# Kernel optimization log

Measured on AMD Instinct MI355X. Metric: run time of the kernel, lower is better.

The kernel has to match this reference:

```python
import jax, jax.numpy as jnp
import numpy as np

DIM = 1024
HEAD_SIZE = 128
B, N = 4, 4096

def setup_inputs() -> dict:
    key = jax.random.key(0)
    kx, kq, kk, kv = jax.random.split(key, 4)
    s = (1.0 / DIM) ** 0.5  # ~ torch Linear init scale
    return {
        "x": jax.random.normal(kx, (B, N, DIM), dtype=jnp.float32),
        "Wq": jax.random.uniform(kq, (HEAD_SIZE, DIM), dtype=jnp.float32, minval=-s, maxval=s),
        "Wk": jax.random.uniform(kk, (HEAD_SIZE, DIM), dtype=jnp.float32, minval=-s, maxval=s),
        "Wv": jax.random.uniform(kv, (HEAD_SIZE, DIM), dtype=jnp.float32, minval=-s, maxval=s),
    }

def reference(x, Wq, Wk, Wv):
    # x: [B, N, dim]; W*: [head_size, dim] (torch Linear convention y = x @ W.T)
    q = jnp.einsum('bnd,hd->bnh', x, Wq)
    k = jnp.einsum('bnd,hd->bnh', x, Wk)
    v = jnp.einsum('bnd,hd->bnh', x, Wv)
    scale = DIM ** (-0.5)  # NOTE: original scales by dim**-0.5, not head_size
    scores = jnp.einsum('bnh,bmh->bnm', q, k) * scale  # [B, N, N]
    weights = jax.nn.softmax(scores, axis=-1)
    context = jnp.einsum('bnm,bmh->bnh', weights, v)  # [B, N, head_size]
    return context
```

## Files before the change

### kernel.cpp

```cpp
#include <hip/hip_runtime.h>

using bf16x8   = __attribute__((ext_vector_type(8))) __bf16;
using f32x4    = __attribute__((ext_vector_type(4))) float;
using floatv4  = __attribute__((ext_vector_type(4))) float;
using ushortv8 = __attribute__((ext_vector_type(8))) unsigned short;

#define N_SEQ 4096
#define N_B   4
#define DIMK  1024
#define HS    128
#define ROWS  (N_B * N_SEQ)
#define KVB   32

__device__ __forceinline__ unsigned short f2bf(float f) {
    unsigned u = __builtin_bit_cast(unsigned, f);
    u += 0x7FFFu + ((u >> 16) & 1u);
    return (unsigned short)(u >> 16);
}

__device__ __forceinline__ void gload16(const unsigned short* g, unsigned short* l) {
    __builtin_amdgcn_global_load_lds(
        (const __attribute__((address_space(1))) unsigned int*)g,
        (__attribute__((address_space(3))) unsigned int*)l, 16, 0, 0);
}

__global__ __launch_bounds__(256) void cast_kernel(
    const float* __restrict__ X,
    const float* __restrict__ Wq,
    const float* __restrict__ Wk,
    const float* __restrict__ Wv,
    unsigned short* __restrict__ Xb,
    unsigned short* __restrict__ Wb)
{
    const int blk = blockIdx.x;
    const float* src;
    unsigned short* dst;
    size_t off;
    if (blk < 8192) {
        src = X; dst = Xb; off = (size_t)blk * 2048;
    } else {
        int wblk = blk - 8192;
        int z = wblk >> 6;
        src = (z == 0) ? Wq : (z == 1) ? Wk : Wv;
        dst = Wb + (size_t)z * (HS * DIMK);
        off = (size_t)(wblk & 63) * 2048;
    }
    size_t i = off + (size_t)threadIdx.x * 8;
    floatv4 a = *reinterpret_cast<const floatv4*>(src + i);
    floatv4 b = *reinterpret_cast<const floatv4*>(src + i + 4);
    ushortv8 o = { f2bf(a.x), f2bf(a.y), f2bf(a.z), f2bf(a.w),
                   f2bf(b.x), f2bf(b.y), f2bf(b.z), f2bf(b.w) };
    *reinterpret_cast<ushortv8*>(dst + i) = o;
}

__global__ __launch_bounds__(256, 3) void proj_kernel(
    const unsigned short* __restrict__ Xb,
    const unsigned short* __restrict__ Wb,
    unsigned short* __restrict__ Qb,
    unsigned short* __restrict__ Kb,
    unsigned short* __restrict__ Vt)
{
    const int z = blockIdx.y;
    const unsigned short* __restrict__ Wz = Wb + (size_t)z * (HS * DIMK);
    const int row0 = blockIdx.x * 64;
    __shared__ unsigned short smem[2 * 64 * 64 + 2 * 128 * 64];
    unsigned short* Xs0 = smem;
    unsigned short* Ws0 = smem + 2 * 64 * 64;
    const int tid = threadIdx.x;
    const int wv = tid >> 6, lane = tid & 63;
    const int lr = lane & 15, lg = lane >> 4;

    f32x4 acc[4][2] = {};

    auto stage = [&](int buf, int k0) {
        #pragma unroll
        for (int i = 0; i < 2; ++i) {
            int g = wv * 2 + i;
            int r = g * 8 + (lane >> 3);
            int sp = (lane & 7) ^ (r & 7);
            gload16(Xb + (size_t)(row0 + r) * DIMK + k0 + sp * 8,
                    Xs0 + buf * (64 * 64) + g * 8 * 64);
        }
        #pragma unroll
        for (int i = 0; i < 4; ++i) {
            int g = wv * 4 + i;
            int r = g * 8 + (lane >> 3);
            int sp = (lane & 7) ^ (r & 7);
            gload16(Wz + (size_t)r * DIMK + k0 + sp * 8,
                    Ws0 + buf * (128 * 64) + g * 8 * 64);
        }
    };

    stage(0, 0);
    __syncthreads();
    for (int ks = 0; ks < DIMK / 64; ++ks) {
        const int cur = ks & 1;
        if (ks < DIMK / 64 - 1) stage(cur ^ 1, (ks + 1) * 64);
        const unsigned short* Xc = Xs0 + cur * (64 * 64);
        const unsigned short* Wc = Ws0 + cur * (128 * 64);
        bf16x8 af[4][2], bfr[2][2];
        #pragma unroll
        for (int mi = 0; mi < 4; ++mi)
            #pragma unroll
            for (int kk = 0; kk < 2; ++kk)
                af[mi][kk] = *reinterpret_cast<const bf16x8*>(
                    &Xc[(mi * 16 + lr) * 64 + (((kk * 4 + lg) ^ (lr & 7)) * 8)]);
        #pragma unroll
        for (int ni = 0; ni < 2; ++ni)
            #pragma unroll
            for (int kk = 0; kk < 2; ++kk)
                bfr[ni][kk] = *reinterpret_cast<const bf16x8*>(
                    &Wc[(wv * 32 + ni * 16 + lr) * 64 + (((kk * 4 + lg) ^ (lr & 7)) * 8)]);
        #pragma unroll
        for (int kk = 0; kk < 2; ++kk)
            #pragma unroll
            for (int mi = 0; mi < 4; ++mi)
                #pragma unroll
                for (int ni = 0; ni < 2; ++ni)
                    acc[mi][ni] = __builtin_amdgcn_mfma_f32_16x16x32_bf16(
                        af[mi][kk], bfr[ni][kk], acc[mi][ni], 0, 0, 0);
        __syncthreads();
    }

    if (z < 2) {
        unsigned short* O = (z == 0) ? Qb : Kb;
        #pragma unroll
        for (int mi = 0; mi < 4; ++mi) {
            int rowb = row0 + mi * 16 + lg * 4;
            #pragma unroll
            for (int ni = 0; ni < 2; ++ni) {
                int col = wv * 32 + ni * 16 + lr;
                #pragma unroll
                for (int r = 0; r < 4; ++r)
                    O[(size_t)(rowb + r) * HS + col] = f2bf(acc[mi][ni][r]);
            }
        }
    } else {
        unsigned short* Cs = smem;
        #pragma unroll
        for (int mi = 0; mi < 4; ++mi)
            #pragma unroll
            for (int ni = 0; ni < 2; ++ni)
                #pragma unroll
                for (int r = 0; r < 4; ++r)
                    Cs[(mi * 16 + lg * 4 + r) * 132 + wv * 32 + ni * 16 + lr] = f2bf(acc[mi][ni][r]);
        __syncthreads();
        const int b  = row0 >> 12;
        const int n0 = row0 & (N_SEQ - 1);
        #pragma unroll
        for (int i = 0; i < 4; ++i) {
            int idx = tid + i * 256;
            int d = idx >> 3, c8 = idx & 7;
            ushortv8 v;
            #pragma unroll
            for (int j = 0; j < 8; ++j)
                v[j] = Cs[(c8 * 8 + j) * 132 + d];
            *reinterpret_cast<ushortv8*>(Vt + (size_t)b * HS * N_SEQ + (size_t)d * N_SEQ + n0 + c8 * 8) = v;
        }
    }
}

__global__ __launch_bounds__(256, 2) void attn_kernel(
    const unsigned short* __restrict__ Qb,
    const unsigned short* __restrict__ Kb,
    const unsigned short* __restrict__ Vt,
    float* __restrict__ part,
    float* __restrict__ plsum,
    int S)
{
    const int qblk  = blockIdx.x;
    const int split = blockIdx.y;
    const int tid = threadIdx.x;
    const int wv = tid >> 6, lane = tid & 63;
    const int lr = lane & 15, lg = lane >> 4;
    const int b    = qblk >> 5;
    const int row0 = (qblk & 31) * 128 + wv * 32;

    __shared__ unsigned short Ks[2][KVB * 128];
    __shared__ unsigned short Vs[2][128 * KVB];
    __shared__ unsigned short Ps[4][32 * 40];
    unsigned short* ps = Ps[wv];

    bf16x8 qf[2][4];
    #pragma unroll
    for (int m = 0; m < 2; ++m) {
        const unsigned short* qp = Qb + ((size_t)b * N_SEQ + row0 + m * 16 + lr) * HS + lg * 8;
        #pragma unroll
        for (int kk = 0; kk < 4; ++kk)
            qf[m][kk] = *reinterpret_cast<const bf16x8*>(qp + kk * 32);
    }

    const int kvlen = N_SEQ / S;
    const int nt = kvlen / KVB;
    const int kv_begin = split * kvlen;
    const unsigned short* Kbb = Kb + (size_t)b * N_SEQ * HS;
    const unsigned short* Vbb = Vt + (size_t)b * HS * N_SEQ;

    auto stage = [&](int buf, int kv0) {
        #pragma unroll
        for (int i = 0; i < 2; ++i) {
            int g = wv * 2 + i;
            int r = g * 4 + (lane >> 4);
            int sp = (lane & 15) ^ (r & 7);
            gload16(Kbb + (size_t)(kv0 + r) * HS + sp * 8, &Ks[buf][g * 4 * 128]);
        }
        #pragma unroll
        for (int i = 0; i < 2; ++i) {
            int g = wv * 2 + i;
            int r = g * 16 + (lane >> 2);
            int sp = (lane & 3) ^ ((r >> 1) & 3);
            gload16(Vbb + (size_t)r * N_SEQ + kv0 + sp * 8, &Vs[buf][g * 16 * KVB]);
        }
    };

    f32x4 ctx[2][8] = {};
    f32x4 lacc[2] = {};
    const ushortv8 ones_u = {0x3F80,0x3F80,0x3F80,0x3F80,0x3F80,0x3F80,0x3F80,0x3F80};
    const bf16x8 onesf = __builtin_bit_cast(bf16x8, ones_u);
    const float CEXP = 0.045084220027780106f;

    stage(0, kv_begin);
    __syncthreads();
    for (int t = 0; t < nt; ++t) {
        const int cur = t & 1;
        if (t + 1 < nt) stage(cur ^ 1, kv_begin + (t + 1) * KVB);

        #pragma unroll
        for (int ni = 0; ni < 2; ++ni) {
            bf16x8 kf[4];
            #pragma unroll
            for (int kk = 0; kk < 4; ++kk)
                kf[kk] = *reinterpret_cast<const bf16x8*>(
                    &Ks[cur][(ni * 16 + lr) * 128 + (((kk * 4 + lg) ^ (lr & 7)) * 8)]);
            #pragma unroll
            for (int m = 0; m < 2; ++m) {
                f32x4 sv = {0.f, 0.f, 0.f, 0.f};
                #pragma unroll
                for (int kk = 0; kk < 4; ++kk)
                    sv = __builtin_amdgcn_mfma_f32_16x16x32_bf16(qf[m][kk], kf[kk], sv, 0, 0, 0);
                #pragma unroll
                for (int r = 0; r < 4; ++r) {
                    float pe = exp2f(sv[r] * CEXP);
                    ps[(m * 16 + lg * 4 + r) * 40 + ni * 16 + lr] = f2bf(pe);
                }
            }
        }

        bf16x8 pf0 = *reinterpret_cast<const bf16x8*>(&ps[lr * 40 + lg * 8]);
        bf16x8 pf1 = *reinterpret_cast<const bf16x8*>(&ps[(16 + lr) * 40 + lg * 8]);
        lacc[0] = __builtin_amdgcn_mfma_f32_16x16x32_bf16(pf0, onesf, lacc[0], 0, 0, 0);
        lacc[1] = __builtin_amdgcn_mfma_f32_16x16x32_bf16(pf1, onesf, lacc[1], 0, 0, 0);
        #pragma unroll
        for (int di = 0; di < 8; ++di) {
            bf16x8 vf = *reinterpret_cast<const bf16x8*>(
                &Vs[cur][(di * 16 + lr) * KVB + ((lg ^ ((lr >> 1) & 3)) * 8)]);
            ctx[0][di] = __builtin_amdgcn_mfma_f32_16x16x32_bf16(pf0, vf, ctx[0][di], 0, 0, 0);
            ctx[1][di] = __builtin_amdgcn_mfma_f32_16x16x32_bf16(pf1, vf, ctx[1][di], 0, 0, 0);
        }
        __syncthreads();
    }

    #pragma unroll
    for (int m = 0; m < 2; ++m) {
        const int qt = b * 256 + (qblk & 31) * 8 + wv * 2 + m;
        const size_t pidx = (size_t)qt * S + split;
        float* pp = part + pidx * (16 * 128);
        #pragma unroll
        for (int r = 0; r < 4; ++r)
            #pragma unroll
            for (int di = 0; di < 8; ++di)
                pp[(lg * 4 + r) * 128 + di * 16 + lr] = ctx[m][di][r];
        if (lr == 0) {
            #pragma unroll
            for (int r = 0; r < 4; ++r)
                plsum[pidx * 16 + lg * 4 + r] = lacc[m][r];
        }
    }
}

__global__ __launch_bounds__(256) void reduce_kernel(
    const float* __restrict__ part,
    const float* __restrict__ plsum,
    float* __restrict__ out, int S)
{
    const int id = blockIdx.x * 256 + threadIdx.x;
    const int d4 = (id & 31) * 4;
    const int grow = id >> 5;
    const int qt = grow >> 4, r16 = grow & 15;
    f32x4 c = {0.f, 0.f, 0.f, 0.f};
    float l = 0.f;
    for (int s = 0; s < S; ++s) {
        f32x4 pv = *reinterpret_cast<const f32x4*>(
            &part[(((size_t)qt * S + s) * 16 + r16) * 128 + d4]);
        c += pv;
        l += plsum[((size_t)qt * S + s) * 16 + r16];
    }
    float inv = 1.0f / l;
    f32x4 o = { c[0]*inv, c[1]*inv, c[2]*inv, c[3]*inv };
    *reinterpret_cast<f32x4*>(&out[(size_t)id * 4]) = o;
}

extern "C" void kernel_launch(void* const* d_in, const int* in_sizes, int n_in,
                              void* d_out, int out_size, void* d_ws, size_t ws_size,
                              hipStream_t stream) {
    const float* x  = (const float*)d_in[0];
    const float* wq = (const float*)d_in[1];
    const float* wk = (const float*)d_in[2];
    const float* wv = (const float*)d_in[3];

    unsigned short* Xb = (unsigned short*)d_ws;
    unsigned short* Wb = Xb + (size_t)ROWS * DIMK;
    unsigned short* Qb = Wb + (size_t)3 * HS * DIMK;
    unsigned short* Kb = Qb + (size_t)ROWS * HS;
    unsigned short* Vt = Kb + (size_t)ROWS * HS;
    float* plsum = (float*)(Vt + (size_t)N_B * HS * N_SEQ);
    float* part  = (float*)d_ws;

    const size_t base = ((size_t)ROWS * DIMK + 3 * HS * DIMK + 3 * (size_t)ROWS * HS) * 2;
    int S;
    if      (ws_size >= base + 4 * (size_t)1024 * 16 * 4) S = 4;
    else if (ws_size >= base + 2 * (size_t)1024 * 16 * 4) S = 2;
    else                                                  S = 1;

    cast_kernel<<<8192 + 192, 256, 0, stream>>>(x, wq, wk, wv, Xb, Wb);
    proj_kernel<<<dim3(256, 3), 256, 0, stream>>>(Xb, Wb, Qb, Kb, Vt);
    attn_kernel<<<dim3(128, S), 256, 0, stream>>>(Qb, Kb, Vt, part, plsum, S);
    reduce_kernel<<<(ROWS * HS) / 1024, 256, 0, stream>>>(part, plsum, (float*)d_out, S);
}
```

Measured before the change: 100.8 us.

## Switch attention to 32x32 MFMA with register-resident P and bf16 partials

Rewrites the attention inner loop to use 32x32x16 bf16 MFMA computing S^T, so the exponentiated probabilities are packed with v_cvt_pk_bf16_f32 and rearranged via v_permlane32_swap in registers instead of going through LDS. Partial context outputs are stored as bf16 rather than fp32 to halve write and read traffic in the split-K reduce. Occupancy hint rises to 3 blocks per CU and the split count can reach 8. The trade-offs are extra rounding error from storing partials in bf16 and more reduce passes when S is larger.

```diff
diff --git a/kernel.cpp b/kernel.cpp
--- a/kernel.cpp
+++ b/kernel.cpp
@@ -2,8 +2,11 @@
 
 using bf16x8   = __attribute__((ext_vector_type(8))) __bf16;
 using f32x4    = __attribute__((ext_vector_type(4))) float;
+using f32x16   = __attribute__((ext_vector_type(16))) float;
 using floatv4  = __attribute__((ext_vector_type(4))) float;
+using ushortv4 = __attribute__((ext_vector_type(4))) unsigned short;
 using ushortv8 = __attribute__((ext_vector_type(8))) unsigned short;
+using uintv4   = __attribute__((ext_vector_type(4))) unsigned int;
 
 #define N_SEQ 4096
 #define N_B   4
@@ -16,6 +19,12 @@
     unsigned u = __builtin_bit_cast(unsigned, f);
     u += 0x7FFFu + ((u >> 16) & 1u);
     return (unsigned short)(u >> 16);
+}
+
+__device__ __forceinline__ unsigned cvtpk(float lo, float hi) {
+    unsigned r;
+    asm("v_cvt_pk_bf16_f32 %0, %1, %2" : "=v"(r) : "v"(lo), "v"(hi));
+    return r;
 }
 
 __device__ __forceinline__ void gload16(const unsigned short* g, unsigned short* l) {
@@ -160,11 +169,11 @@
     }
 }
 
-__global__ __launch_bounds__(256, 2) void attn_kernel(
+__global__ __launch_bounds__(256, 3) void attn_kernel(
     const unsigned short* __restrict__ Qb,
     const unsigned short* __restrict__ Kb,
     const unsigned short* __restrict__ Vt,
-    float* __restrict__ part,
+    unsigned short* __restrict__ part,
     float* __restrict__ plsum,
     int S)
 {
@@ -172,22 +181,19 @@
     const int split = blockIdx.y;
     const int tid = threadIdx.x;
     const int wv = tid >> 6, lane = tid & 63;
-    const int lr = lane & 15, lg = lane >> 4;
+    const int l31 = lane & 31, h = lane >> 5;
     const int b    = qblk >> 5;
     const int row0 = (qblk & 31) * 128 + wv * 32;
 
     __shared__ unsigned short Ks[2][KVB * 128];
     __shared__ unsigned short Vs[2][128 * KVB];
-    __shared__ unsigned short Ps[4][32 * 40];
-    unsigned short* ps = Ps[wv];
-
-    bf16x8 qf[2][4];
-    #pragma unroll
-    for (int m = 0; m < 2; ++m) {
-        const unsigned short* qp = Qb + ((size_t)b * N_SEQ + row0 + m * 16 + lr) * HS + lg * 8;
-        #pragma unroll
-        for (int kk = 0; kk < 4; ++kk)
-            qf[m][kk] = *reinterpret_cast<const bf16x8*>(qp + kk * 32);
+
+    bf16x8 qf[8];
+    {
+        const unsigned short* qp = Qb + ((size_t)b * N_SEQ + row0 + l31) * HS + h * 8;
+        #pragma unroll
+        for (int kk = 0; kk < 8; ++kk)
+            qf[kk] = *reinterpret_cast<const bf16x8*>(qp + kk * 16);
     }
 
     const int kvlen = N_SEQ / S;
@@ -213,8 +219,8 @@
         }
     };
 
-    f32x4 ctx[2][8] = {};
-    f32x4 lacc[2] = {};
+    f32x16 ctx[4] = {};
+    f32x16 lacc = {};
     const ushortv8 ones_u = {0x3F80,0x3F80,0x3F80,0x3F80,0x3F80,0x3F80,0x3F80,0x3F80};
     const bf16x8 onesf = __builtin_bit_cast(bf16x8, ones_u);
     const float CEXP = 0.045084220027780106f;
@@ -225,79 +231,92 @@
         const int cur = t & 1;
         if (t + 1 < nt) stage(cur ^ 1, kv_begin + (t + 1) * KVB);
 
-        #pragma unroll
-        for (int ni = 0; ni < 2; ++ni) {
-            bf16x8 kf[4];
-            #pragma unroll
-            for (int kk = 0; kk < 4; ++kk)
-                kf[kk] = *reinterpret_cast<const bf16x8*>(
-                    &Ks[cur][(ni * 16 + lr) * 128 + (((kk * 4 + lg) ^ (lr & 7)) * 8)]);
-            #pragma unroll
-            for (int m = 0; m < 2; ++m) {
-                f32x4 sv = {0.f, 0.f, 0.f, 0.f};
-                #pragma unroll
-                for (int kk = 0; kk < 4; ++kk)
-                    sv = __builtin_amdgcn_mfma_f32_16x16x32_bf16(qf[m][kk], kf[kk], sv, 0, 0, 0);
-                #pragma unroll
-                for (int r = 0; r < 4; ++r) {
-                    float pe = exp2f(sv[r] * CEXP);
-                    ps[(m * 16 + lg * 4 + r) * 40 + ni * 16 + lr] = f2bf(pe);
-                }
-            }
-        }
-
-        bf16x8 pf0 = *reinterpret_cast<const bf16x8*>(&ps[lr * 40 + lg * 8]);
-        bf16x8 pf1 = *reinterpret_cast<const bf16x8*>(&ps[(16 + lr) * 40 + lg * 8]);
-        lacc[0] = __builtin_amdgcn_mfma_f32_16x16x32_bf16(pf0, onesf, lacc[0], 0, 0, 0);
-        lacc[1] = __builtin_amdgcn_mfma_f32_16x16x32_bf16(pf1, onesf, lacc[1], 0, 0, 0);
-        #pragma unroll
-        for (int di = 0; di < 8; ++di) {
-            bf16x8 vf = *reinterpret_cast<const bf16x8*>(
-                &Vs[cur][(di * 16 + lr) * KVB + ((lg ^ ((lr >> 1) & 3)) * 8)]);
-            ctx[0][di] = __builtin_amdgcn_mfma_f32_16x16x32_bf16(pf0, vf, ctx[0][di], 0, 0, 0);
-            ctx[1][di] = __builtin_amdgcn_mfma_f32_16x16x32_bf16(pf1, vf, ctx[1][di], 0, 0, 0);
+        f32x16 st = {};
+        #pragma unroll
+        for (int kk = 0; kk < 8; ++kk) {
+            bf16x8 kf = *reinterpret_cast<const bf16x8*>(
+                &Ks[cur][l31 * 128 + (((kk * 2 + h) ^ (l31 & 7)) * 8)]);
+            st = __builtin_amdgcn_mfma_f32_32x32x16_bf16(kf, qf[kk], st, 0, 0, 0);
+        }
+
+        float p[16];
+        #pragma unroll
+        for (int r = 0; r < 16; ++r)
+            p[r] = exp2f(st[r] * CEXP);
+
+        bf16x8 pf[2];
+        #pragma unroll
+        for (int half = 0; half < 2; ++half) {
+            unsigned a = cvtpk(p[half*8 + 0], p[half*8 + 1]);
+            unsigned bq = cvtpk(p[half*8 + 2], p[half*8 + 3]);
+            unsigned c = cvtpk(p[half*8 + 4], p[half*8 + 5]);
+            unsigned d = cvtpk(p[half*8 + 6], p[half*8 + 7]);
+            asm("v_permlane32_swap_b32 %0, %1" : "+v"(a), "+v"(c));
+            asm("v_permlane32_swap_b32 %0, %1" : "+v"(bq), "+v"(d));
+            uintv4 w = { a, bq, c, d };
+            pf[half] = __builtin_bit_cast(bf16x8, w);
+        }
+
+        lacc = __builtin_amdgcn_mfma_f32_32x32x16_bf16(pf[0], onesf, lacc, 0, 0, 0);
+        lacc = __builtin_amdgcn_mfma_f32_32x32x16_bf16(pf[1], onesf, lacc, 0, 0, 0);
+
+        #pragma unroll
+        for (int dt = 0; dt < 4; ++dt) {
+            int d = dt * 32 + l31;
+            bf16x8 vf0 = *reinterpret_cast<const bf16x8*>(
+                &Vs[cur][d * KVB + (((0 + h) ^ ((d >> 1) & 3)) * 8)]);
+            ctx[dt] = __builtin_amdgcn_mfma_f32_32x32x16_bf16(pf[0], vf0, ctx[dt], 0, 0, 0);
+            bf16x8 vf1 = *reinterpret_cast<const bf16x8*>(
+                &Vs[cur][d * KVB + (((2 + h) ^ ((d >> 1) & 3)) * 8)]);
+            ctx[dt] = __builtin_amdgcn_mfma_f32_32x32x16_bf16(pf[1], vf1, ctx[dt], 0, 0, 0);
         }
         __syncthreads();
     }
 
+    const int qt = qblk * 4 + wv;
+    unsigned short* pp = part + ((size_t)qt * S + split) * (32 * 128);
     #pragma unroll
-    for (int m = 0; m < 2; ++m) {
-        const int qt = b * 256 + (qblk & 31) * 8 + wv * 2 + m;
-        const size_t pidx = (size_t)qt * S + split;
-        float* pp = part + pidx * (16 * 128);
-        #pragma unroll
-        for (int r = 0; r < 4; ++r)
-            #pragma unroll
-            for (int di = 0; di < 8; ++di)
-                pp[(lg * 4 + r) * 128 + di * 16 + lr] = ctx[m][di][r];
-        if (lr == 0) {
-            #pragma unroll
-            for (int r = 0; r < 4; ++r)
-                plsum[pidx * 16 + lg * 4 + r] = lacc[m][r];
-        }
+    for (int rp = 0; rp < 4; ++rp)
+        #pragma unroll
+        for (int rq = 0; rq < 4; ++rq) {
+            const int r = rp * 4 + rq;
+            const int q = rq + 8 * rp + 4 * h;
+            #pragma unroll
+            for (int dt = 0; dt < 4; ++dt)
+                pp[q * 128 + dt * 32 + l31] = (unsigned short)(cvtpk(ctx[dt][r], ctx[dt][r]) & 0xFFFFu);
+        }
+    if (l31 == 0) {
+        float* pl = plsum + ((size_t)qt * S + split) * 32;
+        #pragma unroll
+        for (int rp = 0; rp < 4; ++rp)
+            #pragma unroll
+            for (int rq = 0; rq < 4; ++rq)
+                pl[rq + 8 * rp + 4 * h] = lacc[rp * 4 + rq];
     }
 }
 
 __global__ __launch_bounds__(256) void reduce_kernel(
-    const float* __restrict__ part,
+    const unsigned short* __restrict__ part,
     const float* __restrict__ plsum,
     float* __restrict__ out, int S)
 {
     const int id = blockIdx.x * 256 + threadIdx.x;
     const int d4 = (id & 31) * 4;
     const int grow = id >> 5;
-    const int qt = grow >> 4, r16 = grow & 15;
+    const int qt = grow >> 5, q = grow & 31;
     f32x4 c = {0.f, 0.f, 0.f, 0.f};
     float l = 0.f;
     for (int s = 0; s < S; ++s) {
-        f32x4 pv = *reinterpret_cast<const f32x4*>(
-            &part[(((size_t)qt * S + s) * 16 + r16) * 128 + d4]);
-        c += pv;
-        l += plsum[((size_t)qt * S + s) * 16 + r16];
+        ushortv4 pv = *reinterpret_cast<const ushortv4*>(
+            &part[(((size_t)qt * S + s) * 32 + q) * 128 + d4]);
+        #pragma unroll
+        for (int j = 0; j < 4; ++j)
+            c[j] += __builtin_bit_cast(float, (unsigned)pv[j] << 16);
+        l += plsum[((size_t)qt * S + s) * 32 + q];
     }
     float inv = 1.0f / l;
     f32x4 o = { c[0]*inv, c[1]*inv, c[2]*inv, c[3]*inv };
-    *reinterpret_cast<f32x4*>(&out[(size_t)id * 4]) = o;
+    *reinterpret_cast<f32x4*>(&out[(size_t)grow * 128 + d4]) = o;
 }
 
 extern "C" void kernel_launch(void* const* d_in, const int* in_sizes, int n_in,
@@ -314,13 +333,14 @@
     unsigned short* Kb = Qb + (size_t)ROWS * HS;
     unsigned short* Vt = Kb + (size_t)ROWS * HS;
     float* plsum = (float*)(Vt + (size_t)N_B * HS * N_SEQ);
-    float* part  = (float*)d_ws;
+    unsigned short* part = (unsigned short*)d_ws;
 
     const size_t base = ((size_t)ROWS * DIMK + 3 * HS * DIMK + 3 * (size_t)ROWS * HS) * 2;
     int S;
-    if      (ws_size >= base + 4 * (size_t)1024 * 16 * 4) S = 4;
-    else if (ws_size >= base + 2 * (size_t)1024 * 16 * 4) S = 2;
-    else                                                  S = 1;
+    if      (ws_size >= base + 8 * (size_t)512 * 32 * 4) S = 8;
+    else if (ws_size >= base + 4 * (size_t)512 * 32 * 4) S = 4;
+    else if (ws_size >= base + 2 * (size_t)512 * 32 * 4) S = 2;
+    else                                                 S = 1;
 
     cast_kernel<<<8192 + 192, 256, 0, stream>>>(x, wq, wk, wv, Xb, Wb);
     proj_kernel<<<dim3(256, 3), 256, 0, stream>>>(Xb, Wb, Qb, Kb, Vt);
```

Result: faster. 94.06 us (-6.7%).
